# Kernel tuning notes

Hardware: AMD Instinct MI355X
Metric: run time of the kernel (lower is better)

The kernel has to match this reference:

```python
import jax, jax.numpy as jnp
import numpy as np

N, E, F_IN, H, G = 100000, 3200000, 128, 256, 64


def gcn_layer(x, src, dst, W, b, n):
    # GCNConv with added self-loops and symmetric normalization:
    # out = D^{-1/2} (A + I) D^{-1/2} X W + b
    h = x @ W  # [n, H]
    deg = jax.ops.segment_sum(jnp.ones_like(dst, dtype=h.dtype), dst, num_segments=n) + 1.0
    dinv = jax.lax.rsqrt(deg)
    coef = dinv[src] * dinv[dst]  # [E]
    agg = jax.ops.segment_sum(h[src] * coef[:, None], dst, num_segments=n)
    out = agg + h * (dinv * dinv)[:, None]  # self-loop term: 1/deg
    return out + b


def global_mean_pool(x, batch, num_graphs):
    sums = jax.ops.segment_sum(x, batch, num_segments=num_graphs)
    cnts = jax.ops.segment_sum(jnp.ones((x.shape[0],), x.dtype), batch, num_segments=num_graphs)
    return sums / jnp.maximum(cnts, 1.0)[:, None]


def conv_pass(x, edge_index, batch, params):
    (W0, b0, W1, b1, W2, b2, lin0_W, lin0_b) = params
    src, dst = edge_index[0], edge_index[1]
    n = x.shape[0]
    x = jax.nn.relu(gcn_layer(x, src, dst, W0, b0, n))
    x = jax.nn.relu(gcn_layer(x, src, dst, W1, b1, n))
    x = gcn_layer(x, src, dst, W2, b2, n)
    x = global_mean_pool(x, batch, G)
    # dropout(p=0.5) is identity in eval mode
    return x @ lin0_W + lin0_b  # [G, H/2]


def setup_inputs() -> dict:
    key = jax.random.key(0)
    ks = jax.random.split(key, 20)
    d = {}
    for i, nm in enumerate(['x0', 'x1', 'x2']):
        d[nm] = jax.random.normal(ks[i], (N, F_IN), dtype=jnp.float32)
    for i, nm in enumerate(['edge_index0', 'edge_index1', 'edge_index2']):
        d[nm] = jax.random.randint(ks[3 + i], (2, E), 0, N, dtype=jnp.int32)
    for i, nm in enumerate(['batch0', 'batch1', 'batch2']):
        d[nm] = jnp.sort(jax.random.randint(ks[6 + i], (N,), 0, G, dtype=jnp.int32))
    s = lambda fan: 1.0 / np.sqrt(fan)
    d['W0'] = jax.random.uniform(ks[9], (F_IN, H), jnp.float32, -s(F_IN), s(F_IN))
    d['b0'] = jnp.zeros((H,), jnp.float32)
    d['W1'] = jax.random.uniform(ks[10], (H, H), jnp.float32, -s(H), s(H))
    d['b1'] = jnp.zeros((H,), jnp.float32)
    d['W2'] = jax.random.uniform(ks[11], (H, H), jnp.float32, -s(H), s(H))
    d['b2'] = jnp.zeros((H,), jnp.float32)
    d['lin0_W'] = jax.random.uniform(ks[12], (H, H // 2), jnp.float32, -s(H), s(H))
    d['lin0_b'] = jax.random.uniform(ks[13], (H // 2,), jnp.float32, -s(H), s(H))
    d['lin_W'] = jax.random.uniform(ks[14], (H, 1), jnp.float32, -s(H), s(H))
    d['lin_b'] = jax.random.uniform(ks[15], (1,), jnp.float32, -s(H), s(H))
    return d


def reference(x0, x1, x2, edge_index0, edge_index1, edge_index2,
              batch0, batch1, batch2,
              W0, b0, W1, b1, W2, b2, lin0_W, lin0_b, lin_W, lin_b):
    params = (W0, b0, W1, b1, W2, b2, lin0_W, lin0_b)
    z0 = conv_pass(x0, edge_index0, batch0, params)
    z1 = conv_pass(x1, edge_index1, batch1, params)
    z2 = conv_pass(x2, edge_index2, batch2, params)
    EPS = 1e-6  # torch F.pairwise_distance eps
    dist_p = jnp.linalg.norm(z0 - z1 + EPS, axis=1)
    dist_n = jnp.linalg.norm(z0 - z2 + EPS, axis=1)
    y1 = jnp.concatenate([z0, z1], axis=1) @ lin_W + lin_b
    y2 = jnp.concatenate([z0, z2], axis=1) @ lin_W + lin_b
    score_p = jax.nn.sigmoid(y1)
    score_n = jax.nn.sigmoid(y2)
    correct = jnp.sum(dist_n - dist_p > 0).astype(jnp.int32).reshape(1)
    correct_score = jnp.sum(score_p - score_n > 0).astype(jnp.int32).reshape(1)
    return (z0, z1, z2, correct, score_p, score_n, correct_score)
```

## Files before the change

### kernel.cpp

```cpp
#include <hip/hip_runtime.h>
#include <math.h>

#define NN 100000
#define EE 3200000

typedef __attribute__((ext_vector_type(8))) short bf16x8;
typedef __attribute__((ext_vector_type(4))) float f32x4;

__device__ __forceinline__ unsigned short f2b(float f) {
  unsigned u = __float_as_uint(f);
  u += 0x7fffu + ((u >> 16) & 1u);
  return (unsigned short)(u >> 16);
}
__device__ __forceinline__ float b2f(unsigned short s) {
  return __uint_as_float(((unsigned)s) << 16);
}
__device__ __forceinline__ float blo(unsigned u) { return __uint_as_float(u << 16); }
__device__ __forceinline__ float bhi(unsigned u) { return __uint_as_float(u & 0xffff0000u); }
__device__ __forceinline__ unsigned pack2(float lo, float hi) {
  return ((unsigned)f2b(hi) << 16) | (unsigned)f2b(lo);
}

#define WPB 8192
#define NODES_PER_PASS 16384
#define NPASS 7
#define HB 64

__global__ void zero_int(int* __restrict__ p, int n) {
  int i = blockIdx.x * 256 + threadIdx.x;
  if (i < n) p[i] = 0;
}

__global__ __launch_bounds__(256) void hist_part(
    const int* __restrict__ d0, const int* __restrict__ d1, const int* __restrict__ d2,
    unsigned* __restrict__ partials) {
  __shared__ unsigned cnt[WPB];
  int b = blockIdx.x, p = blockIdx.y, g = blockIdx.z;
  const int* dst = (g == 0) ? d0 : (g == 1) ? d1 : d2;
  for (int i = threadIdx.x; i < WPB; i += 256) cnt[i] = 0;
  __syncthreads();
  unsigned lo = (unsigned)(p * NODES_PER_PASS);
  int base = b * (EE / HB);
  int end = base + EE / HB;
  for (int i = base + threadIdx.x * 4; i < end; i += 256 * 4) {
    int4 d = *(const int4*)(dst + i);
    unsigned n0 = (unsigned)d.x - lo;
    unsigned n1 = (unsigned)d.y - lo;
    unsigned n2 = (unsigned)d.z - lo;
    unsigned n3 = (unsigned)d.w - lo;
    if (n0 < NODES_PER_PASS) atomicAdd(&cnt[n0 >> 1], 1u << ((n0 & 1) * 16));
    if (n1 < NODES_PER_PASS) atomicAdd(&cnt[n1 >> 1], 1u << ((n1 & 1) * 16));
    if (n2 < NODES_PER_PASS) atomicAdd(&cnt[n2 >> 1], 1u << ((n2 & 1) * 16));
    if (n3 < NODES_PER_PASS) atomicAdd(&cnt[n3 >> 1], 1u << ((n3 & 1) * 16));
  }
  __syncthreads();
  unsigned* out = partials + ((size_t)((g * NPASS + p) * HB + b)) * WPB;
  for (int i = threadIdx.x; i < WPB; i += 256) out[i] = cnt[i];
}

__global__ void hist_reduce(const unsigned* __restrict__ partials,
                            unsigned* __restrict__ deg3w) {
  int i = blockIdx.x * 256 + threadIdx.x;
  int p = blockIdx.y, g = blockIdx.z;
  unsigned s = 0;
  const unsigned* base = partials + ((size_t)((g * NPASS + p) * HB)) * WPB + i;
#pragma unroll 16
  for (int b = 0; b < HB; ++b) s += base[(size_t)b * WPB];
  int word = p * WPB + i;
  if (word < NN / 2) deg3w[(size_t)g * (NN / 2) + word] = s;
}

__global__ void calc_dinv3(const unsigned short* __restrict__ deg3u,
                           float* __restrict__ dinv3, int n3) {
  int i = blockIdx.x * 256 + threadIdx.x;
  if (i < n3) dinv3[i] = 1.0f / sqrtf((float)(deg3u[i] + 1));
}

#define SCHUNK 1024
#define NCHUNK 98

__global__ __launch_bounds__(256) void scan_part(const unsigned short* __restrict__ deg3u,
                                                 int* __restrict__ bsum) {
  int c = blockIdx.x, g = blockIdx.y;
  const unsigned short* deg = deg3u + (size_t)g * NN;
  int base = c * SCHUNK;
  int s = 0;
  for (int i = threadIdx.x; i < SCHUNK; i += 256) {
    int idx = base + i;
    s += (idx < NN) ? (int)deg[idx] : 0;
  }
#pragma unroll
  for (int o = 32; o; o >>= 1) s += __shfl_down(s, o, 64);
  __shared__ int ws[4];
  if ((threadIdx.x & 63) == 0) ws[threadIdx.x >> 6] = s;
  __syncthreads();
  if (threadIdx.x == 0) bsum[g * NCHUNK + c] = ws[0] + ws[1] + ws[2] + ws[3];
}

__global__ __launch_bounds__(128) void scan_mid(int* __restrict__ bsum) {
  int g = blockIdx.x;
  int t = threadIdx.x;
  int v = (t < NCHUNK) ? bsum[g * NCHUNK + t] : 0;
  int lane = t & 63, wv = t >> 6;
  int x = v;
#pragma unroll
  for (int o = 1; o < 64; o <<= 1) {
    int tt = __shfl_up(x, o, 64);
    if (lane >= o) x += tt;
  }
  __shared__ int w0sum;
  if (wv == 0 && lane == 63) w0sum = x;
  __syncthreads();
  int excl = x - v + (wv ? w0sum : 0);
  if (t < NCHUNK) bsum[g * NCHUNK + t] = excl;
}

__global__ __launch_bounds__(1024) void scan_final(const unsigned short* __restrict__ deg3u,
    const int* __restrict__ bsum, int* __restrict__ offs3) {
  int c = blockIdx.x, g = blockIdx.y;
  const unsigned short* deg = deg3u + (size_t)g * NN;
  int* offs = offs3 + (size_t)g * (NN + 1);
  int t = threadIdx.x;
  int idx = c * SCHUNK + t;
  int v = (idx < NN) ? (int)deg[idx] : 0;
  int lane = t & 63, wv = t >> 6;
  int x = v;
#pragma unroll
  for (int o = 1; o < 64; o <<= 1) {
    int tt = __shfl_up(x, o, 64);
    if (lane >= o) x += tt;
  }
  __shared__ int ws[16];
  if (lane == 63) ws[wv] = x;
  __syncthreads();
  int woff = 0;
  for (int j = 0; j < wv; ++j) woff += ws[j];
  if (idx < NN) offs[idx] = bsum[g * NCHUNK + c] + woff + x - v;
  if (idx == NN - 1) offs[NN] = EE;
}

__global__ void fill_csr(const int* __restrict__ src, const int* __restrict__ dst,
                         const int* __restrict__ offs,
                         int* __restrict__ fillc, int* __restrict__ ent,
                         int e) {
  int i = blockIdx.x * 256 + threadIdx.x;
  if (i >= e) return;
  int d = dst[i], s = src[i];
  int pos = offs[d] + atomicAdd(&fillc[d], 1);
  ent[pos] = s;
}

__global__ void conv_bf(const float* __restrict__ in, unsigned* __restrict__ out, int n4) {
  int i = blockIdx.x * 256 + threadIdx.x;
  if (i >= n4) return;
  float4 v = ((const float4*)in)[i];
  ((uint2*)out)[i] = make_uint2(pack2(v.x, v.y), pack2(v.z, v.w));
}

__global__ void conv_wt(const float* __restrict__ W, unsigned short* __restrict__ Wt, int K) {
  int i = blockIdx.x * 256 + threadIdx.x;
  if (i >= 256 * K) return;
  int nn = i / K, kk = i - nn * K;
  Wt[i] = f2b(W[(size_t)kk * 256 + nn]);
}

__global__ __launch_bounds__(256) void agg256_bf(const unsigned short* __restrict__ x,
    const int* __restrict__ ent, const int* __restrict__ offs,
    const float* __restrict__ dinv, unsigned short* __restrict__ y, int n) {
  int v = (blockIdx.x * 256 + threadIdx.x) >> 6;
  v = __builtin_amdgcn_readfirstlane(v);
  int lane = threadIdx.x & 63;
  if (v >= n) return;
  float dv = dinv[v];
  const uint2* selfp = (const uint2*)(x + ((size_t)(unsigned)v << 8)) + lane;
  uint2 self = *selfp;
  float a0 = dv * blo(self.x), a1 = dv * bhi(self.x);
  float a2 = dv * blo(self.y), a3 = dv * bhi(self.y);
  int s = offs[v], e = offs[v + 1];
  int i = s;
#define ACC4(rr, ww) { \
    a0 += ww * blo(rr.x); a1 += ww * bhi(rr.x); \
    a2 += ww * blo(rr.y); a3 += ww * bhi(rr.y); }
  for (; i + 7 < e; i += 8) {
    int s0 = ent[i],     s1 = ent[i + 1], s2 = ent[i + 2], s3 = ent[i + 3];
    int s4 = ent[i + 4], s5 = ent[i + 5], s6 = ent[i + 6], s7 = ent[i + 7];
    float w0 = dinv[s0], w1 = dinv[s1], w2 = dinv[s2], w3 = dinv[s3];
    float w4 = dinv[s4], w5 = dinv[s5], w6 = dinv[s6], w7 = dinv[s7];
    uint2 r0 = *((const uint2*)(x + ((size_t)(unsigned)s0 << 8)) + lane);
    uint2 r1 = *((const uint2*)(x + ((size_t)(unsigned)s1 << 8)) + lane);
    uint2 r2 = *((const uint2*)(x + ((size_t)(unsigned)s2 << 8)) + lane);
    uint2 r3 = *((const uint2*)(x + ((size_t)(unsigned)s3 << 8)) + lane);
    uint2 r4 = *((const uint2*)(x + ((size_t)(unsigned)s4 << 8)) + lane);
    uint2 r5 = *((const uint2*)(x + ((size_t)(unsigned)s5 << 8)) + lane);
    uint2 r6 = *((const uint2*)(x + ((size_t)(unsigned)s6 << 8)) + lane);
    uint2 r7 = *((const uint2*)(x + ((size_t)(unsigned)s7 << 8)) + lane);
    ACC4(r0, w0); ACC4(r1, w1); ACC4(r2, w2); ACC4(r3, w3);
    ACC4(r4, w4); ACC4(r5, w5); ACC4(r6, w6); ACC4(r7, w7);
  }
  for (; i + 3 < e; i += 4) {
    int s0 = ent[i], s1 = ent[i + 1], s2 = ent[i + 2], s3 = ent[i + 3];
    float w0 = dinv[s0], w1 = dinv[s1], w2 = dinv[s2], w3 = dinv[s3];
    uint2 r0 = *((const uint2*)(x + ((size_t)(unsigned)s0 << 8)) + lane);
    uint2 r1 = *((const uint2*)(x + ((size_t)(unsigned)s1 << 8)) + lane);
    uint2 r2 = *((const uint2*)(x + ((size_t)(unsigned)s2 << 8)) + lane);
    uint2 r3 = *((const uint2*)(x + ((size_t)(unsigned)s3 << 8)) + lane);
    ACC4(r0, w0); ACC4(r1, w1); ACC4(r2, w2); ACC4(r3, w3);
  }
  for (; i < e; ++i) {
    int s0 = ent[i];
    float w0 = dinv[s0];
    uint2 r0 = *((const uint2*)(x + ((size_t)(unsigned)s0 << 8)) + lane);
    ACC4(r0, w0);
  }
#undef ACC4
  uint2* yp = (uint2*)(y + ((size_t)(unsigned)v << 8)) + lane;
  *yp = make_uint2(pack2(dv * a0, dv * a1), pack2(dv * a2, dv * a3));
}

__global__ __launch_bounds__(256) void agg128_bf(const unsigned short* __restrict__ x,
    const int* __restrict__ ent, const int* __restrict__ offs,
    const float* __restrict__ dinv, unsigned short* __restrict__ y, int n) {
  int v = (blockIdx.x * 256 + threadIdx.x) >> 6;
  v = __builtin_amdgcn_readfirstlane(v);
  int lane = threadIdx.x & 63;
  if (v >= n) return;
  float dv = dinv[v];
  const unsigned* selfp = (const unsigned*)(x + ((size_t)(unsigned)v << 7)) + lane;
  unsigned self = *selfp;
  float a0 = dv * blo(self), a1 = dv * bhi(self);
  int s = offs[v], e = offs[v + 1];
  int i = s;
#define ACC2(rr, ww) { a0 += ww * blo(rr); a1 += ww * bhi(rr); }
  for (; i + 7 < e; i += 8) {
    int s0 = ent[i],     s1 = ent[i + 1], s2 = ent[i + 2], s3 = ent[i + 3];
    int s4 = ent[i + 4], s5 = ent[i + 5], s6 = ent[i + 6], s7 = ent[i + 7];
    float w0 = dinv[s0], w1 = dinv[s1], w2 = dinv[s2], w3 = dinv[s3];
    float w4 = dinv[s4], w5 = dinv[s5], w6 = dinv[s6], w7 = dinv[s7];
    unsigned r0 = *((const unsigned*)(x + ((size_t)(unsigned)s0 << 7)) + lane);
    unsigned r1 = *((const unsigned*)(x + ((size_t)(unsigned)s1 << 7)) + lane);
    unsigned r2 = *((const unsigned*)(x + ((size_t)(unsigned)s2 << 7)) + lane);
    unsigned r3 = *((const unsigned*)(x + ((size_t)(unsigned)s3 << 7)) + lane);
    unsigned r4 = *((const unsigned*)(x + ((size_t)(unsigned)s4 << 7)) + lane);
    unsigned r5 = *((const unsigned*)(x + ((size_t)(unsigned)s5 << 7)) + lane);
    unsigned r6 = *((const unsigned*)(x + ((size_t)(unsigned)s6 << 7)) + lane);
    unsigned r7 = *((const unsigned*)(x + ((size_t)(unsigned)s7 << 7)) + lane);
    ACC2(r0, w0); ACC2(r1, w1); ACC2(r2, w2); ACC2(r3, w3);
    ACC2(r4, w4); ACC2(r5, w5); ACC2(r6, w6); ACC2(r7, w7);
  }
  for (; i + 3 < e; i += 4) {
    int s0 = ent[i], s1 = ent[i + 1], s2 = ent[i + 2], s3 = ent[i + 3];
    float w0 = dinv[s0], w1 = dinv[s1], w2 = dinv[s2], w3 = dinv[s3];
    unsigned r0 = *((const unsigned*)(x + ((size_t)(unsigned)s0 << 7)) + lane);
    unsigned r1 = *((const unsigned*)(x + ((size_t)(unsigned)s1 << 7)) + lane);
    unsigned r2 = *((const unsigned*)(x + ((size_t)(unsigned)s2 << 7)) + lane);
    unsigned r3 = *((const unsigned*)(x + ((size_t)(unsigned)s3 << 7)) + lane);
    ACC2(r0, w0); ACC2(r1, w1); ACC2(r2, w2); ACC2(r3, w3);
  }
  for (; i < e; ++i) {
    int s0 = ent[i];
    float w0 = dinv[s0];
    unsigned r0 = *((const unsigned*)(x + ((size_t)(unsigned)s0 << 7)) + lane);
    ACC2(r0, w0);
  }
#undef ACC2
  unsigned* yp = (unsigned*)(y + ((size_t)(unsigned)v << 7)) + lane;
  *yp = pack2(dv * a0, dv * a1);
}

#define LDA 40
__global__ __launch_bounds__(256) void gemm_mfma(
    const unsigned short* __restrict__ A, const unsigned short* __restrict__ Bt,
    const float* __restrict__ bias, unsigned short* __restrict__ C,
    int M, int K, int do_relu) {
  __shared__ unsigned short As[128 * LDA];
  __shared__ unsigned short Bs[128 * LDA];
  int tid = threadIdx.x;
  int row0 = blockIdx.x * 128;
  int col0 = blockIdx.y * 128;
  int wave = tid >> 6, lane = tid & 63;
  int wm = wave >> 1, wn = wave & 1;
  int lr = lane & 15, quad = lane >> 4;

  f32x4 acc[4][4];
#pragma unroll
  for (int i = 0; i < 4; ++i)
#pragma unroll
    for (int j = 0; j < 4; ++j) acc[i][j] = (f32x4){0.f, 0.f, 0.f, 0.f};

  for (int k0 = 0; k0 < K; k0 += 32) {
#pragma unroll
    for (int p = 0; p < 2; ++p) {
      int i = tid + p * 256;
      int r = i >> 2, q = i & 3;
      int row = row0 + r; if (row >= M) row = M - 1;
      uint4 va = *(const uint4*)(A + (size_t)row * K + k0 + q * 8);
      *(uint4*)&As[r * LDA + q * 8] = va;
      uint4 vb = *(const uint4*)(Bt + (size_t)(col0 + r) * K + k0 + q * 8);
      *(uint4*)&Bs[r * LDA + q * 8] = vb;
    }
    __syncthreads();
    bf16x8 af[4], bf[4];
#pragma unroll
    for (int mi = 0; mi < 4; ++mi)
      af[mi] = *(const bf16x8*)&As[(wm * 64 + mi * 16 + lr) * LDA + quad * 8];
#pragma unroll
    for (int ni = 0; ni < 4; ++ni)
      bf[ni] = *(const bf16x8*)&Bs[(wn * 64 + ni * 16 + lr) * LDA + quad * 8];
#pragma unroll
    for (int mi = 0; mi < 4; ++mi)
#pragma unroll
      for (int ni = 0; ni < 4; ++ni)
        acc[mi][ni] = __builtin_amdgcn_mfma_f32_16x16x32_bf16(af[mi], bf[ni], acc[mi][ni], 0, 0, 0);
    __syncthreads();
  }

  float bv[4];
#pragma unroll
  for (int ni = 0; ni < 4; ++ni) bv[ni] = bias[col0 + wn * 64 + ni * 16 + lr];
#pragma unroll
  for (int mi = 0; mi < 4; ++mi) {
#pragma unroll
    for (int r = 0; r < 4; ++r) {
      int grow = row0 + wm * 64 + mi * 16 + quad * 4 + r;
      if (grow < M) {
#pragma unroll
        for (int ni = 0; ni < 4; ++ni) {
          float v = acc[mi][ni][r] + bv[ni];
          if (do_relu) v = fmaxf(v, 0.f);
          C[(size_t)grow * 256 + col0 + wn * 64 + ni * 16 + lr] = f2b(v);
        }
      }
    }
  }
}

__global__ __launch_bounds__(256) void pool_sum_bf(const unsigned short* __restrict__ h,
    const int* __restrict__ batch, float* __restrict__ sums,
    float* __restrict__ cnts, int n) {
  int f = threadIdx.x;
  int v0 = blockIdx.x * 128;
  if (v0 >= n) return;
  int vend = min(v0 + 128, n);
  int cur = batch[v0];
  float acc = 0.f;
  int cnt = 0;
  for (int v = v0; v < vend; ++v) {
    int b = batch[v];
    if (b != cur) {
      atomicAdd(&sums[cur * 256 + f], acc);
      if (f == 0) atomicAdd(&cnts[cur], (float)cnt);
      acc = 0.f; cnt = 0; cur = b;
    }
    acc += b2f(h[(size_t)v * 256 + f]);
    cnt++;
  }
  atomicAdd(&sums[cur * 256 + f], acc);
  if (f == 0) atomicAdd(&cnts[cur], (float)cnt);
}

__global__ __launch_bounds__(256) void pool_lin2(const float* __restrict__ sums,
    const float* __restrict__ cnts, const float* __restrict__ W2,
    const float* __restrict__ b2, const float* __restrict__ lin0W,
    const float* __restrict__ lin0b, float* __restrict__ z) {
  int g = blockIdx.x, t = threadIdx.x;
  __shared__ float s[256], u[256];
  float inv = 1.0f / fmaxf(cnts[g], 1.0f);
  s[t] = sums[g * 256 + t] * inv;
  __syncthreads();
  float acc = b2[t];
  for (int j = 0; j < 256; ++j) acc += s[j] * W2[j * 256 + t];
  u[t] = acc;
  __syncthreads();
  if (t < 128) {
    float a2 = lin0b[t];
    for (int k = 0; k < 256; ++k) a2 += u[k] * lin0W[k * 128 + t];
    z[g * 128 + t] = a2;
  }
}

__global__ __launch_bounds__(64) void final_triplet(const float* __restrict__ z,
    const float* __restrict__ lin_W, const float* __restrict__ lin_b,
    float* __restrict__ out) {
  int g = threadIdx.x;
  const float* z0 = z;
  const float* z1 = z + 8192;
  const float* z2 = z + 16384;
  float dp = 0.f, dn = 0.f;
  float y1 = lin_b[0], y2 = lin_b[0];
  for (int f = 0; f < 128; ++f) {
    float a = z0[g * 128 + f], b = z1[g * 128 + f], c = z2[g * 128 + f];
    float d1 = a - b + 1e-6f, d2 = a - c + 1e-6f;
    dp += d1 * d1; dn += d2 * d2;
    float w0 = lin_W[f], w1 = lin_W[128 + f];
    y1 += a * w0 + b * w1;
    y2 += a * w0 + c * w1;
  }
  dp = sqrtf(dp); dn = sqrtf(dn);
  float sp = 1.f / (1.f + expf(-y1));
  float sn = 1.f / (1.f + expf(-y2));
  out[24577 + g] = sp;
  out[24641 + g] = sn;
  unsigned long long m1 = __ballot(dn - dp > 0.f);
  unsigned long long m2 = __ballot(sp - sn > 0.f);
  if (g == 0) {
    out[24576] = (float)__popcll(m1);
    out[24705] = (float)__popcll(m2);
  }
}

extern "C" void kernel_launch(void* const* d_in, const int* in_sizes, int n_in,
                              void* d_out, int out_size, void* d_ws, size_t ws_size,
                              hipStream_t stream) {
  const float* xin[3]  = {(const float*)d_in[0], (const float*)d_in[1], (const float*)d_in[2]};
  const int* ei[3]     = {(const int*)d_in[3], (const int*)d_in[4], (const int*)d_in[5]};
  const int* batch[3]  = {(const int*)d_in[6], (const int*)d_in[7], (const int*)d_in[8]};
  const float* W0 = (const float*)d_in[9],  *b0 = (const float*)d_in[10];
  const float* W1 = (const float*)d_in[11], *b1 = (const float*)d_in[12];
  const float* W2 = (const float*)d_in[13], *b2 = (const float*)d_in[14];
  const float* lin0W = (const float*)d_in[15], *lin0b = (const float*)d_in[16];
  const float* linW  = (const float*)d_in[17], *linb  = (const float*)d_in[18];
  float* out = (float*)d_out;

  unsigned short* ybf = (unsigned short*)d_ws;
  unsigned short* hbf = ybf + (size_t)NN * 256;
  unsigned short* xbf = hbf + (size_t)NN * 256;
  int* ent = (int*)(xbf + (size_t)NN * 128);
  unsigned short* Wt0 = (unsigned short*)(ent + EE);
  unsigned short* Wt1 = Wt0 + 256 * 128;
  int* fillc3 = (int*)(Wt1 + 256 * 256);
  float* sums3 = (float*)(fillc3 + 3 * NN);
  float* cnts3 = sums3 + 3 * 64 * 256;
  int zero_elems = 3 * NN + 3 * 64 * 256 + 3 * 64;
  float* dinv3 = cnts3 + 3 * 64;
  int* offs3 = (int*)(dinv3 + 3 * NN);
  unsigned* deg3w = (unsigned*)(offs3 + 3 * (NN + 1));
  int* bsum = (int*)(deg3w + 3 * (NN / 2));
  unsigned* partials = (unsigned*)ybf;
  const unsigned short* deg3u = (const unsigned short*)deg3w;

  const int EB = (EE + 255) / 256;
  dim3 ggrid((NN + 127) / 128, 2);

  conv_wt<<<(256 * 128 + 255) / 256, 256, 0, stream>>>(W0, Wt0, 128);
  conv_wt<<<(256 * 256 + 255) / 256, 256, 0, stream>>>(W1, Wt1, 256);

  zero_int<<<(zero_elems + 255) / 256, 256, 0, stream>>>(fillc3, zero_elems);
  hist_part<<<dim3(HB, NPASS, 3), 256, 0, stream>>>(ei[0] + EE, ei[1] + EE, ei[2] + EE, partials);
  hist_reduce<<<dim3(WPB / 256, NPASS, 3), 256, 0, stream>>>(partials, deg3w);
  calc_dinv3<<<(3 * NN + 255) / 256, 256, 0, stream>>>(deg3u, dinv3, 3 * NN);
  scan_part<<<dim3(NCHUNK, 3), 256, 0, stream>>>(deg3u, bsum);
  scan_mid<<<3, 128, 0, stream>>>(bsum);
  scan_final<<<dim3(NCHUNK, 3), 1024, 0, stream>>>(deg3u, bsum, offs3);

  for (int g = 0; g < 3; ++g) {
    const int* src = ei[g];
    const int* dst = ei[g] + EE;
    const float* dinv = dinv3 + (size_t)g * NN;
    const int* offs = offs3 + (size_t)g * (NN + 1);

    fill_csr<<<EB, 256, 0, stream>>>(src, dst, offs, fillc3 + (size_t)g * NN, ent, EE);

    conv_bf<<<(NN * 128 / 4 + 255) / 256, 256, 0, stream>>>(xin[g], (unsigned*)xbf, NN * 128 / 4);

    agg128_bf<<<(NN + 3) / 4, 256, 0, stream>>>(xbf, ent, offs, dinv, ybf, NN);
    gemm_mfma<<<ggrid, 256, 0, stream>>>(ybf, Wt0, b0, hbf, NN, 128, 1);
    agg256_bf<<<(NN + 3) / 4, 256, 0, stream>>>(hbf, ent, offs, dinv, ybf, NN);
    gemm_mfma<<<ggrid, 256, 0, stream>>>(ybf, Wt1, b1, hbf, NN, 256, 1);
    agg256_bf<<<(NN + 3) / 4, 256, 0, stream>>>(hbf, ent, offs, dinv, ybf, NN);

    pool_sum_bf<<<(NN + 127) / 128, 256, 0, stream>>>(ybf, batch[g],
        sums3 + (size_t)g * 64 * 256, cnts3 + (size_t)g * 64, NN);
    pool_lin2<<<64, 256, 0, stream>>>(sums3 + (size_t)g * 64 * 256, cnts3 + (size_t)g * 64,
        W2, b2, lin0W, lin0b, out + g * 8192);
  }

  final_triplet<<<1, 64, 0, stream>>>(out, linW, linb, out);
}
```

Measured before the change: 2.823 ms.

## Fold last GCN aggregation into pooling via per-node graph-weight coefficients

Replaces the third 256-wide edge aggregation and the mean-pool sum with an algebraic rewrite. For each source node it computes coefficients c[u,g], the summed normalized edge weights into graph g, using atomics over the edges plus a self-loop term. A weighted reduction over node features and a partial-sum reduce then produce the pooled sums directly. This avoids gathering 256 features per edge, at the cost of 3.2M scalar atomics into a 25.6MB buffer and a low-occupancy wpool kernel with 64 accumulators per thread.

```diff
diff --git a/kernel.cpp b/kernel.cpp
--- a/kernel.cpp
+++ b/kernel.cpp
@@ -334,28 +334,60 @@
   }
 }
 
-__global__ __launch_bounds__(256) void pool_sum_bf(const unsigned short* __restrict__ h,
-    const int* __restrict__ batch, float* __restrict__ sums,
+__global__ void calc_c(const int* __restrict__ src, const int* __restrict__ dst,
+                       const int* __restrict__ batch, const float* __restrict__ dinv,
+                       float* __restrict__ c, int e) {
+  int i = blockIdx.x * 256 + threadIdx.x;
+  if (i >= e) return;
+  int s = src[i], d = dst[i];
+  int g = batch[d];
+  atomicAdd(&c[((size_t)(unsigned)s << 6) + g], dinv[s] * dinv[d]);
+}
+
+__global__ __launch_bounds__(256) void self_cnt(const int* __restrict__ batch,
+    const float* __restrict__ dinv, float* __restrict__ c,
     float* __restrict__ cnts, int n) {
-  int f = threadIdx.x;
-  int v0 = blockIdx.x * 128;
-  if (v0 >= n) return;
-  int vend = min(v0 + 128, n);
-  int cur = batch[v0];
-  float acc = 0.f;
-  int cnt = 0;
-  for (int v = v0; v < vend; ++v) {
-    int b = batch[v];
-    if (b != cur) {
-      atomicAdd(&sums[cur * 256 + f], acc);
-      if (f == 0) atomicAdd(&cnts[cur], (float)cnt);
-      acc = 0.f; cnt = 0; cur = b;
-    }
-    acc += b2f(h[(size_t)v * 256 + f]);
-    cnt++;
-  }
-  atomicAdd(&sums[cur * 256 + f], acc);
-  if (f == 0) atomicAdd(&cnts[cur], (float)cnt);
+  __shared__ unsigned hh[64];
+  if (threadIdx.x < 64) hh[threadIdx.x] = 0;
+  __syncthreads();
+  int u = blockIdx.x * 256 + threadIdx.x;
+  if (u < n) {
+    int g = batch[u];
+    atomicAdd(&hh[g], 1u);
+    float dv = dinv[u];
+    c[((size_t)(unsigned)u << 6) + g] += dv * dv;
+  }
+  __syncthreads();
+  if (threadIdx.x < 64 && hh[threadIdx.x])
+    atomicAdd(&cnts[threadIdx.x], (float)hh[threadIdx.x]);
+}
+
+#define WB 256
+__global__ __launch_bounds__(256) void wpool(const unsigned short* __restrict__ h,
+    const float* __restrict__ c, float* __restrict__ partial, int n) {
+  int b = blockIdx.x, f = threadIdx.x;
+  int per = (n + WB - 1) / WB;
+  int u0 = b * per, u1 = min(u0 + per, n);
+  float acc[64];
+#pragma unroll
+  for (int g = 0; g < 64; ++g) acc[g] = 0.f;
+  for (int u = u0; u < u1; ++u) {
+    float hv = b2f(h[((size_t)(unsigned)u << 8) + f]);
+    const float* cu = c + ((size_t)(unsigned)u << 6);
+#pragma unroll
+    for (int g = 0; g < 64; ++g) acc[g] = fmaf(cu[g], hv, acc[g]);
+  }
+  float* out = partial + ((size_t)b << 14);
+#pragma unroll
+  for (int g = 0; g < 64; ++g) out[g * 256 + f] = acc[g];
+}
+
+__global__ __launch_bounds__(256) void wreduce(const float* __restrict__ partial,
+                                               float* __restrict__ sums) {
+  int g = blockIdx.x, f = threadIdx.x;
+  float s = 0.f;
+  for (int b = 0; b < WB; ++b) s += partial[((size_t)b << 14) + g * 256 + f];
+  sums[g * 256 + f] = s;
 }
 
 __global__ __launch_bounds__(256) void pool_lin2(const float* __restrict__ sums,
@@ -436,6 +468,8 @@
   unsigned* deg3w = (unsigned*)(offs3 + 3 * (NN + 1));
   int* bsum = (int*)(deg3w + 3 * (NN / 2));
   unsigned* partials = (unsigned*)ybf;
+  float* cbuf = (float*)ybf;
+  float* wpart = cbuf + (size_t)NN * 64;
   const unsigned short* deg3u = (const unsigned short*)deg3w;
 
   const int EB = (EE + 255) / 256;
@@ -466,10 +500,13 @@
     gemm_mfma<<<ggrid, 256, 0, stream>>>(ybf, Wt0, b0, hbf, NN, 128, 1);
     agg256_bf<<<(NN + 3) / 4, 256, 0, stream>>>(hbf, ent, offs, dinv, ybf, NN);
     gemm_mfma<<<ggrid, 256, 0, stream>>>(ybf, Wt1, b1, hbf, NN, 256, 1);
-    agg256_bf<<<(NN + 3) / 4, 256, 0, stream>>>(hbf, ent, offs, dinv, ybf, NN);
-
-    pool_sum_bf<<<(NN + 127) / 128, 256, 0, stream>>>(ybf, batch[g],
-        sums3 + (size_t)g * 64 * 256, cnts3 + (size_t)g * 64, NN);
+
+    zero_int<<<(NN * 64 + 255) / 256, 256, 0, stream>>>((int*)cbuf, NN * 64);
+    calc_c<<<EB, 256, 0, stream>>>(src, dst, batch[g], dinv, cbuf, EE);
+    self_cnt<<<(NN + 255) / 256, 256, 0, stream>>>(batch[g], dinv, cbuf,
+        cnts3 + (size_t)g * 64, NN);
+    wpool<<<WB, 256, 0, stream>>>(hbf, cbuf, wpart, NN);
+    wreduce<<<64, 256, 0, stream>>>(wpart, sums3 + (size_t)g * 64 * 256);
     pool_lin2<<<64, 256, 0, stream>>>(sums3 + (size_t)g * 64 * 256, cnts3 + (size_t)g * 64,
         W2, b2, lin0W, lin0b, out + g * 8192);
   }
```

Result: slower. 3.054 ms (+8.2%).
